# Kernel optimization log

Measured on AMD Instinct MI355X. Metric: run time of the kernel, lower is better.

The kernel has to match this reference:

```python
import jax, jax.numpy as jnp
import numpy as np

NUM_HEADS = 8
KEY_DIM = 32   # head_dim * attn_ratio(=1.0); head_dim = 256 // 8
SCALE = KEY_DIM ** -0.5


def qconv(x, w, groups, pad):
    """Quaternion (Hamilton product) conv. x: [B,C,4,H,W], w: [4,O,C//groups,kh,kw]."""
    B, C, Q, H, W = x.shape
    # fold the 4 quaternion components into the batch dim -> one conv per weight component
    xs = jnp.transpose(x, (0, 2, 1, 3, 4)).reshape(B * 4, C, H, W)
    ys = []
    for i in range(4):
        y = jax.lax.conv_general_dilated(
            xs, w[i], (1, 1), [(pad, pad), (pad, pad)],
            dimension_numbers=('NCHW', 'OIHW', 'NCHW'), feature_group_count=groups)
        ys.append(y.reshape(B, 4, y.shape[1], y.shape[2], y.shape[3]))
    yr, yi, yj, yk = ys  # y{w}[:, a] = conv(x_component_a, w_component_w)
    out_r = yr[:, 0] - yi[:, 1] - yj[:, 2] - yk[:, 3]
    out_i = yi[:, 0] + yr[:, 1] + yk[:, 2] - yj[:, 3]
    out_j = yj[:, 0] - yk[:, 1] + yr[:, 2] + yi[:, 3]
    out_k = yk[:, 0] + yj[:, 1] - yi[:, 2] + yr[:, 3]
    return jnp.stack([out_r, out_i, out_j, out_k], axis=2)  # [B,O,4,H,W]


def iqbn(x, gamma, beta, eps=1e-5):
    """Independent quaternion BN: per (channel, component) stats over (B,H,W)."""
    mean = x.mean(axis=(0, 3, 4), keepdims=True)
    var = x.var(axis=(0, 3, 4), keepdims=True)
    g = gamma[None, :, :, None, None]
    b = beta[None, :, :, None, None]
    return g * (x - mean) * jax.lax.rsqrt(var + eps) + b


def psablock(x, w_qkv, w_proj, w_pe, g_n, b_n, w_f1, g_f1, b_f1, w_f2, g_f2, b_f2):
    B, C, Q, H, W = x.shape
    N = H * W
    # --- QAttention ---
    qkv = qconv(x, w_qkv, 1, 0).reshape(B, NUM_HEADS, -1, 4, N)  # [B,nh,2kd+hd,4,N]
    q = qkv[:, :, :KEY_DIM]
    k = qkv[:, :, KEY_DIM:2 * KEY_DIM]
    v = qkv[:, :, 2 * KEY_DIM:]
    # channel attention: gram over spatial tokens N, softmax over channel dim d
    attn = jnp.einsum('bhcqn,bhdqn->bhqcd', q, k) * SCALE
    attn = jax.nn.softmax(attn, axis=-1)
    o = jnp.einsum('bhqcd,bhdqn->bhcqn', attn, v).reshape(B, C, 4, H, W)
    o = o + qconv(o, w_pe, C // 4, 1)   # depthwise-style 3x3 positional conv
    o = qconv(o, w_proj, 1, 0)
    o = iqbn(o, g_n, b_n)
    x = x + o  # shortcut
    # --- conv FFN ---
    f = qconv(x, w_f1, 1, 0)
    f = jax.nn.relu(iqbn(f, g_f1, b_f1))
    f = qconv(f, w_f2, 1, 0)
    f = iqbn(f, g_f2, b_f2)
    return x + f  # shortcut


def setup_inputs() -> dict:
    key = jax.random.key(0)
    ks = jax.random.split(key, 6)
    C, S = 256, 64
    return {
        'x': jax.random.normal(ks[0], (4, C, 4, S, S), jnp.float32),
        'w_qkv': jax.random.normal(ks[1], (4, 3 * C, C, 1, 1), jnp.float32) * 0.05,
        'w_proj': jax.random.normal(ks[2], (4, C, C, 1, 1), jnp.float32) * 0.05,
        'w_pe': jax.random.normal(ks[3], (4, C, 4, 3, 3), jnp.float32) * 0.05,
        'g_n': jnp.ones((C, 4), jnp.float32),
        'b_n': jnp.zeros((C, 4), jnp.float32),
        'w_f1': jax.random.normal(ks[4], (4, 2 * C, C, 1, 1), jnp.float32) * 0.05,
        'g_f1': jnp.ones((2 * C, 4), jnp.float32),
        'b_f1': jnp.zeros((2 * C, 4), jnp.float32),
        'w_f2': jax.random.normal(ks[5], (4, C, 2 * C, 1, 1), jnp.float32) * 0.05,
        'g_f2': jnp.ones((C, 4), jnp.float32),
        'b_f2': jnp.zeros((C, 4), jnp.float32),
    }


def reference(x, w_qkv, w_proj, w_pe, g_n, b_n, w_f1, g_f1, b_f1, w_f2, g_f2, b_f2):
    return psablock(x, w_qkv, w_proj, w_pe, g_n, b_n, w_f1, g_f1, b_f1, w_f2, g_f2, b_f2)
```

## Files before the change

### kernel.cpp

```cpp
#include <hip/hip_runtime.h>

typedef unsigned short u16;
typedef __bf16 bf16x8 __attribute__((ext_vector_type(8)));
typedef float f32x4 __attribute__((ext_vector_type(4)));

typedef const __attribute__((address_space(1))) void gv_t;
typedef __attribute__((address_space(3))) void lv_t;

__device__ __forceinline__ float b2f(u16 u) {
    union { unsigned int i; float f; } v; v.i = ((unsigned int)u) << 16; return v.f;
}
__device__ __forceinline__ u16 f2b(float f) {
    union { unsigned int i; float f; } v; v.f = f;
    unsigned int b = v.i;
    return (u16)((b + 0x7FFFu + ((b >> 16) & 1u)) >> 16);
}

__constant__ int   c_qidx[16] = {0,1,2,3, 1,0,3,2, 2,3,0,1, 3,2,1,0};
__constant__ float c_qsgn[16] = {1,-1,-1,-1, 1,1,1,-1, 1,-1,1,1, 1,1,-1,1};

__device__ __forceinline__ void frag_decode(long i, int KT, int& m, int& k) {
    int j = (int)(i & 7), r16 = (int)((i >> 3) & 15);
    int quad = (int)((i >> 7) & 3), frag = (int)((i >> 9) & 7);
    long t2 = i >> 12;
    int ktile = (int)(t2 % KT), mtile = (int)(t2 / KT);
    m = mtile * 128 + frag * 16 + r16;
    k = ktile * 32 + quad * 8 + j;
}
__device__ __forceinline__ u16 weff(const float* __restrict__ w, int OC, int Cin, int m, int k) {
    int o = m >> 2, p = m & 3, c = k >> 2, q = k & 3, pq = (p << 2) | q;
    return f2b(c_qsgn[pq] * w[c_qidx[pq] * OC + o * Cin + c]);
}

__global__ void build_weights(const float* __restrict__ wqkv, const float* __restrict__ wproj,
                              const float* __restrict__ wf1, const float* __restrict__ wf2,
                              const float* __restrict__ wpe,
                              u16* __restrict__ Wq, u16* __restrict__ Wp, u16* __restrict__ W1,
                              u16* __restrict__ W2, float* __restrict__ Wpe_eff)
{
    long i = (long)blockIdx.x * 256 + threadIdx.x;
    int m, k;
    if (i < 3145728L) {
        frag_decode(i, 32, m, k);
        Wq[i] = weff(wqkv, 196608, 256, m, k);
        return;
    }
    i -= 3145728L;
    if (i < 1048576L) {
        frag_decode(i, 32, m, k);
        Wp[i] = weff(wproj, 65536, 256, m, k);
        return;
    }
    i -= 1048576L;
    if (i < 2097152L) {
        frag_decode(i, 32, m, k);
        W1[i] = weff(wf1, 131072, 256, m, k);
        return;
    }
    i -= 2097152L;
    if (i < 2097152L) {
        frag_decode(i, 64, m, k);
        W2[i] = weff(wf2, 131072, 512, m, k);
        return;
    }
    i -= 2097152L;
    if (i < 147456L) {
        int g = (int)(i / 2304), r = (int)(i % 2304);
        int tap = r >> 8, r2 = r & 255;
        int fi = r2 >> 4, of = r2 & 15;
        int ol = of >> 2, p = of & 3, ci = fi >> 2, q = fi & 3, pq = (p << 2) | q;
        Wpe_eff[i] = c_qsgn[pq] * wpe[c_qidx[pq] * 9216 + (g * 4 + ol) * 36 + ci * 9 + tap];
    }
}

__global__ void zero_f(float* __restrict__ a)
{
    a[blockIdx.x * 256 + threadIdx.x] = 0.f;
}

__global__ __launch_bounds__(256) void cast_tr(const float* __restrict__ x, u16* __restrict__ Xt)
{
    int b = blockIdx.z, mt = blockIdx.y * 64, nt = blockIdx.x * 64;
    __shared__ u16 tl[64][66];
    int t = threadIdx.x, sub = t >> 4, c4 = (t & 15) * 4;
#pragma unroll
    for (int rr = 0; rr < 4; rr++) {
        int row = rr * 16 + sub;
        float4 v = *(const float4*)(x + ((long)b * 1024 + mt + row) * 4096 + nt + c4);
        uint2 pk;
        pk.x = (unsigned int)f2b(v.x) | ((unsigned int)f2b(v.y) << 16);
        pk.y = (unsigned int)f2b(v.z) | ((unsigned int)f2b(v.w) << 16);
        *(uint2*)(&tl[row][c4]) = pk;
    }
    __syncthreads();
#pragma unroll
    for (int rr = 0; rr < 4; rr++) {
        int row = rr * 16 + sub;
        uint2 o;
        o.x = (unsigned int)tl[c4][row] | ((unsigned int)tl[c4 + 1][row] << 16);
        o.y = (unsigned int)tl[c4 + 2][row] | ((unsigned int)tl[c4 + 3][row] << 16);
        *(uint2*)(Xt + ((long)b * 4096 + nt + row) * 1024 + mt + c4) = o;
    }
}

__device__ __forceinline__ void gl16(const u16* g, u16* l) {
    __builtin_amdgcn_global_load_lds((gv_t*)g, (lv_t*)l, 16, 0, 0);
}

template<int QM>
__device__ __forceinline__ void load_a(const u16* aS, bf16x8 (&afr)[4][2]) {
#pragma unroll
    for (int f = 0; f < 4; f++)
#pragma unroll
        for (int kk = 0; kk < 2; kk++)
            afr[f][kk] = *(const bf16x8*)(aS + (kk * 8 + QM * 4 + f) * 512);
}
template<int QN>
__device__ __forceinline__ void load_b(const u16* bS, bf16x8 (&bfr)[2][2]) {
#pragma unroll
    for (int g = 0; g < 2; g++)
#pragma unroll
        for (int kk = 0; kk < 2; kk++)
            bfr[g][kk] = *(const bf16x8*)(bS + (QN * 2 + g) * 1024 + kk * 512);
}
template<int QM, int QN>
__device__ __forceinline__ void mf16(const bf16x8 (&afr)[4][2], const bf16x8 (&bfr)[2][2],
                                     f32x4 (&acc)[8][4]) {
    __builtin_amdgcn_s_setprio(1);
#pragma unroll
    for (int f = 0; f < 4; f++)
#pragma unroll
        for (int g = 0; g < 2; g++)
#pragma unroll
            for (int kk = 0; kk < 2; kk++)
                acc[QM * 4 + f][QN * 2 + g] = __builtin_amdgcn_mfma_f32_16x16x32_bf16(
                    afr[f][kk], bfr[g][kk], acc[QM * 4 + f][QN * 2 + g], 0, 0, 0);
    __builtin_amdgcn_s_setprio(0);
}

#define PHASE_SYNC() \
    __builtin_amdgcn_sched_barrier(0); \
    asm volatile("s_waitcnt vmcnt(4)" ::: "memory"); \
    __builtin_amdgcn_s_barrier(); \
    asm volatile("s_waitcnt lgkmcnt(0)" ::: "memory"); \
    __builtin_amdgcn_sched_barrier(0);

template<bool TROUT>
__global__ __launch_bounds__(512, 2) void gemm256(
    const u16* __restrict__ A, const u16* __restrict__ Bt, u16* __restrict__ C,
    int M, int N, int K, long strideB, long strideC)
{
    __shared__ __align__(16) u16 smem[65536];
    const int t = threadIdx.x;
    const int b = blockIdx.z;
    const int m0 = blockIdx.y * 256, n0 = blockIdx.x * 256;
    const int l = t & 63, w = t >> 6;
    const int wr = w >> 2, wc = w & 3;
    const int quad = l >> 4, r16 = l & 15;
    const int KT32 = K >> 5, NT = K >> 6;
    const u16* Bb = Bt + (long)b * strideB;

    const u16* aB0 = A + (long)(2 * blockIdx.y) * KT32 * 4096 + t * 8;
    const u16* aB1 = aB0 + (long)KT32 * 4096;
    const int rowS = (w >> 1) * 16 + r16;
    const int colS = (w & 1) * 32 + quad * 8;
    const u16* bB0 = Bb + (long)(n0 + rowS) * K + colS;
    const u16* bB1 = bB0 + (long)128 * K;
    const long bStep = (long)64 * K;

    const int aOff = wr * 8192 + l * 8;
    const int bOff = 16384 + wc * 4096 + l * 8;

#define STAGE_A(ktv, h) { \
    const u16* s_ = ((h) ? aB1 : aB0) + (long)(ktv) * 8192; \
    u16* d_ = smem + (((ktv) & 1) * 32768) + (h) * 8192 + t * 8; \
    gl16(s_, d_); gl16(s_ + 4096, d_ + 4096); }
#define STAGE_B(ktv, h) { \
    const u16* s_ = ((h) ? bB1 : bB0) + (ktv) * 64; \
    u16* d_ = smem + (((ktv) & 1) * 32768) + 16384 + (h) * 8192 + t * 8; \
    gl16(s_, d_); gl16(s_ + bStep, d_ + 4096); }

    f32x4 acc[8][4];
#pragma unroll
    for (int i = 0; i < 8; i++)
#pragma unroll
        for (int j = 0; j < 4; j++) acc[i][j] = (f32x4){0.f, 0.f, 0.f, 0.f};

    bf16x8 RA[4][2], RB0[2][2], RB1[2][2];

    STAGE_B(0, 0); STAGE_A(0, 0); STAGE_B(0, 1); STAGE_A(0, 1);
    STAGE_B(1, 0); STAGE_A(1, 0);
    asm volatile("s_waitcnt vmcnt(4)" ::: "memory");
    __builtin_amdgcn_s_barrier();

    for (int kt = 0; kt < NT; ++kt) {
        const int so = (kt & 1) * 32768;
        const u16* aS = smem + so + aOff;
        const u16* bS = smem + so + bOff;
        const int k1 = (kt + 1 < NT) ? kt + 1 : NT - 1;
        const int k2 = (kt + 2 < NT) ? kt + 2 : NT - 1;

        load_a<0>(aS, RA);
        load_b<0>(bS, RB0);
        STAGE_B(k1, 1);
        PHASE_SYNC();
        mf16<0, 0>(RA, RB0, acc);
        __builtin_amdgcn_s_barrier();
        load_b<1>(bS, RB1);
        STAGE_A(k1, 1);
        PHASE_SYNC();
        mf16<0, 1>(RA, RB1, acc);
        __builtin_amdgcn_s_barrier();
        load_a<1>(aS, RA);
        STAGE_B(k2, 0);
        PHASE_SYNC();
        mf16<1, 1>(RA, RB1, acc);
        __builtin_amdgcn_s_barrier();
        STAGE_A(k2, 0);
        PHASE_SYNC();
        mf16<1, 0>(RA, RB0, acc);
        __builtin_amdgcn_s_barrier();
    }
    asm volatile("s_waitcnt vmcnt(0)" ::: "memory");
    __builtin_amdgcn_s_barrier();
#undef STAGE_A
#undef STAGE_B

    if (!TROUT) {
        u16* Cb = C + (long)b * strideC;
#pragma unroll
        for (int i = 0; i < 8; i++)
#pragma unroll
            for (int j = 0; j < 4; j++) {
                int mm = m0 + wr * 128 + i * 16 + quad * 4;
                int nn = n0 + wc * 64 + j * 16 + r16;
#pragma unroll
                for (int r = 0; r < 4; r++)
                    Cb[(long)(mm + r) * N + nn] = f2b(acc[i][j][r]);
            }
    } else {
        u16* Ct = smem;
        u16* Cb = C + (long)b * strideC;
#pragma unroll
        for (int h = 0; h < 2; h++) {
            __syncthreads();
            if ((wc >> 1) == h) {
#pragma unroll
                for (int i = 0; i < 8; i++)
#pragma unroll
                    for (int j = 0; j < 4; j++) {
                        int nn = (wc & 1) * 64 + j * 16 + r16;
                        int mm = wr * 128 + i * 16 + quad * 4;
                        ushort4 pk;
                        pk.x = f2b(acc[i][j][0]); pk.y = f2b(acc[i][j][1]);
                        pk.z = f2b(acc[i][j][2]); pk.w = f2b(acc[i][j][3]);
                        *(ushort4*)(Ct + nn * 264 + mm) = pk;
                    }
            }
            __syncthreads();
#pragma unroll
            for (int e = 0; e < 8; e++) {
                int idx = e * 512 + t;
                int n = idx >> 5, m8 = (idx & 31) * 8;
                uint4 v = *(const uint4*)(Ct + n * 264 + m8);
                *(uint4*)(Cb + (long)(n0 + h * 128 + n) * M + m0 + m8) = v;
            }
        }
    }
}
#undef PHASE_SYNC

__global__ __launch_bounds__(256) void attn_s(const u16* __restrict__ QKV, float* __restrict__ S)
{
    const int chunk = blockIdx.x, bhp = blockIdx.y;
    const int bi = bhp >> 5, h = (bhp >> 2) & 7, p = bhp & 3;
    const long rs = 16384;
    const u16* base = QKV + (long)bi * (3072L * 4096) + (long)(h * 384 + p) * 4096;
    const int t = threadIdx.x, l = t & 63, w = t >> 6;
    const int quad = l >> 4, r16 = l & 15;
    __shared__ float Sred[4][32][32];

    f32x4 acc[2][2];
#pragma unroll
    for (int i = 0; i < 2; i++)
#pragma unroll
        for (int j = 0; j < 2; j++) acc[i][j] = (f32x4){0.f, 0.f, 0.f, 0.f};

    const int nb = chunk * 1024 + w * 256 + quad * 8;
    for (int kk = 0; kk < 256; kk += 32) {
        long off = nb + kk;
        bf16x8 q0 = *(const bf16x8*)(base + (long)r16 * rs + off);
        bf16x8 q1 = *(const bf16x8*)(base + (long)(16 + r16) * rs + off);
        bf16x8 k0 = *(const bf16x8*)(base + (long)(32 + r16) * rs + off);
        bf16x8 k1 = *(const bf16x8*)(base + (long)(48 + r16) * rs + off);
        acc[0][0] = __builtin_amdgcn_mfma_f32_16x16x32_bf16(q0, k0, acc[0][0], 0, 0, 0);
        acc[0][1] = __builtin_amdgcn_mfma_f32_16x16x32_bf16(q0, k1, acc[0][1], 0, 0, 0);
        acc[1][0] = __builtin_amdgcn_mfma_f32_16x16x32_bf16(q1, k0, acc[1][0], 0, 0, 0);
        acc[1][1] = __builtin_amdgcn_mfma_f32_16x16x32_bf16(q1, k1, acc[1][1], 0, 0, 0);
    }
#pragma unroll
    for (int i = 0; i < 2; i++)
#pragma unroll
        for (int j = 0; j < 2; j++)
#pragma unroll
            for (int r = 0; r < 4; r++)
                Sred[w][i * 16 + quad * 4 + r][j * 16 + r16] = acc[i][j][r];
    __syncthreads();
    for (int e = t; e < 1024; e += 256) {
        int c = e >> 5, d = e & 31;
        float v = Sred[0][c][d] + Sred[1][c][d] + Sred[2][c][d] + Sred[3][c][d];
        atomicAdd(&S[(long)bhp * 1024 + e], v);
    }
}

__global__ __launch_bounds__(256) void attn_pv(const u16* __restrict__ QKV, const float* __restrict__ S,
                                               u16* __restrict__ O)
{
    const int ns = blockIdx.x * 512, bhp = blockIdx.y;
    const int bi = bhp >> 5, h = (bhp >> 2) & 7, p = bhp & 3;
    const long rs = 16384;
    const u16* base = QKV + (long)bi * (3072L * 4096) + (long)(h * 384 + p) * 4096;
    const int t = threadIdx.x;
    __shared__ float Pl[1024];
    for (int e = t; e < 1024; e += 256) Pl[e] = S[(long)bhp * 1024 + e];
    __syncthreads();
    if (t < 32) {
        float r[32];
        float mx = -1e30f;
#pragma unroll
        for (int d = 0; d < 32; d++) { r[d] = Pl[t * 32 + d] * 0.17677669529663687f; mx = fmaxf(mx, r[d]); }
        float sum = 0.f;
#pragma unroll
        for (int d = 0; d < 32; d++) { r[d] = __expf(r[d] - mx); sum += r[d]; }
        float inv = 1.f / sum;
#pragma unroll
        for (int d = 0; d < 32; d++) Pl[t * 32 + d] = r[d] * inv;
    }
    __syncthreads();

    float v[32][2];
#pragma unroll
    for (int d = 0; d < 32; d++) {
        unsigned int u = *(const unsigned int*)(base + (long)(64 + d) * rs + ns + 2 * t);
        v[d][0] = b2f((u16)u); v[d][1] = b2f((u16)(u >> 16));
    }
    u16* Ob = O + (long)bi * (1024L * 4096) + (long)(h * 128 + p) * 4096;
    for (int c = 0; c < 32; c++) {
        float s0 = 0.f, s1 = 0.f;
        const float4* prow = (const float4*)(&Pl[c * 32]);
#pragma unroll
        for (int dq = 0; dq < 8; dq++) {
            float4 pv = prow[dq];
            s0 = fmaf(pv.x, v[4*dq+0][0], s0); s1 = fmaf(pv.x, v[4*dq+0][1], s1);
            s0 = fmaf(pv.y, v[4*dq+1][0], s0); s1 = fmaf(pv.y, v[4*dq+1][1], s1);
            s0 = fmaf(pv.z, v[4*dq+2][0], s0); s1 = fmaf(pv.z, v[4*dq+2][1], s1);
            s0 = fmaf(pv.w, v[4*dq+3][0], s0); s1 = fmaf(pv.w, v[4*dq+3][1], s1);
        }
        *(unsigned int*)(Ob + (long)c * 16384 + ns + 2 * t) =
            (unsigned int)f2b(s0) | ((unsigned int)f2b(s1) << 16);
    }
}

__global__ __launch_bounds__(256) void pe_kernel(const u16* __restrict__ Oin,
                                                 const float* __restrict__ Wpe,
                                                 u16* __restrict__ O2t)
{
    const int tile = blockIdx.x, g = blockIdx.y, bi = blockIdx.z;
    const int y0 = (tile >> 2) * 16, x0 = (tile & 3) * 16;
    __shared__ float tin[16][324];
    const int t = threadIdx.x;
    const u16* Ob = Oin + (long)bi * (1024L * 4096) + (long)(g * 16) * 4096;
    for (int e = t; e < 16 * 324; e += 256) {
        int f = e / 324, rem = e % 324;
        int yy = rem / 18 - 1 + y0, xx = rem % 18 - 1 + x0;
        float v = 0.f;
        if (yy >= 0 && yy < 64 && xx >= 0 && xx < 64)
            v = b2f(Ob[(long)f * 4096 + yy * 64 + xx]);
        tin[f][rem] = v;
    }
    __syncthreads();
    const int y = t >> 4, x = t & 15;
    float acc[16];
#pragma unroll
    for (int of = 0; of < 16; of++) acc[of] = tin[of][(y + 1) * 18 + (x + 1)];
    const float* Wg = Wpe + g * 2304;
    for (int dy = 0; dy < 3; dy++)
        for (int dx = 0; dx < 3; dx++) {
            int off = (y + dy) * 18 + (x + dx);
            int tap = dy * 3 + dx;
            for (int fi = 0; fi < 16; fi++) {
                float v = tin[fi][off];
                const float* wp = Wg + (tap * 16 + fi) * 16;
#pragma unroll
                for (int of = 0; of < 16; of++) acc[of] = fmaf(wp[of], v, acc[of]);
            }
        }
    long n = (long)(y0 + y) * 64 + (x0 + x);
    unsigned int* op = (unsigned int*)(O2t + ((long)bi * 4096 + n) * 1024 + g * 16);
#pragma unroll
    for (int u = 0; u < 8; u++)
        op[u] = (unsigned int)f2b(acc[2 * u]) | ((unsigned int)f2b(acc[2 * u + 1]) << 16);
}

__global__ __launch_bounds__(256) void bn_stats(const u16* __restrict__ X, float* __restrict__ stats, int M)
{
    const int m = blockIdx.x, t = threadIdx.x;
    float s = 0.f, ss = 0.f;
    for (int b = 0; b < 4; b++) {
        const u16* rowp = X + ((long)b * M + m) * 4096;
        for (int pass = 0; pass < 2; pass++) {
            uint4 uv = *(const uint4*)(rowp + pass * 2048 + t * 8);
            unsigned int wsa[4] = {uv.x, uv.y, uv.z, uv.w};
#pragma unroll
            for (int u = 0; u < 4; u++) {
                float v0 = b2f((u16)wsa[u]), v1 = b2f((u16)(wsa[u] >> 16));
                s += v0 + v1; ss += v0 * v0 + v1 * v1;
            }
        }
    }
    __shared__ float rs[4], rss[4];
    for (int o = 32; o > 0; o >>= 1) { s += __shfl_down(s, o); ss += __shfl_down(ss, o); }
    if ((t & 63) == 0) { rs[t >> 6] = s; rss[t >> 6] = ss; }
    __syncthreads();
    if (t == 0) {
        float S = rs[0] + rs[1] + rs[2] + rs[3];
        float SS = rss[0] + rss[1] + rss[2] + rss[3];
        float mean = S * (1.f / 16384.f);
        float var = SS * (1.f / 16384.f) - mean * mean;
        stats[2 * m] = mean;
        stats[2 * m + 1] = rsqrtf(var + 1e-5f);
    }
}

__global__ __launch_bounds__(256) void bn_add_tr(const float* __restrict__ x, const u16* __restrict__ P,
    const float* __restrict__ stats, const float* __restrict__ gamma, const float* __restrict__ beta,
    u16* __restrict__ X1t)
{
    int b = blockIdx.z, mt = blockIdx.y * 64, nt = blockIdx.x * 64;
    __shared__ u16 tl[64][66];
    int t = threadIdx.x, sub = t >> 4, c4 = (t & 15) * 4;
#pragma unroll
    for (int rr = 0; rr < 4; rr++) {
        int row = rr * 16 + sub, m = mt + row;
        float gm = gamma[m] * stats[2 * m + 1];
        float bs = beta[m] - gm * stats[2 * m];
        long gi = ((long)b * 1024 + m) * 4096 + nt + c4;
        float4 xv = *(const float4*)(x + gi);
        uint2 pv = *(const uint2*)(P + gi);
        uint2 pk;
        pk.x = (unsigned int)f2b(xv.x + fmaf(gm, b2f((u16)pv.x), bs)) |
               ((unsigned int)f2b(xv.y + fmaf(gm, b2f((u16)(pv.x >> 16)), bs)) << 16);
        pk.y = (unsigned int)f2b(xv.z + fmaf(gm, b2f((u16)pv.y), bs)) |
               ((unsigned int)f2b(xv.w + fmaf(gm, b2f((u16)(pv.y >> 16)), bs)) << 16);
        *(uint2*)(&tl[row][c4]) = pk;
    }
    __syncthreads();
#pragma unroll
    for (int rr = 0; rr < 4; rr++) {
        int row = rr * 16 + sub;
        uint2 o;
        o.x = (unsigned int)tl[c4][row] | ((unsigned int)tl[c4 + 1][row] << 16);
        o.y = (unsigned int)tl[c4 + 2][row] | ((unsigned int)tl[c4 + 3][row] << 16);
        *(uint2*)(X1t + ((long)b * 4096 + nt + row) * 1024 + mt + c4) = o;
    }
}

__global__ __launch_bounds__(256) void bn_stats_col(const u16* __restrict__ Xp, float* __restrict__ accum)
{
    const int t = threadIdx.x;
    const int f0 = t * 8;
    float s[8], ss[8];
#pragma unroll
    for (int u = 0; u < 8; u++) { s[u] = 0.f; ss[u] = 0.f; }
    const u16* base = Xp + (long)blockIdx.x * 128 * 2048;
    for (int r = 0; r < 128; r++) {
        uint4 uv = *(const uint4*)(base + (long)r * 2048 + f0);
        unsigned int wsa[4] = {uv.x, uv.y, uv.z, uv.w};
#pragma unroll
        for (int u = 0; u < 4; u++) {
            float v0 = b2f((u16)wsa[u]), v1 = b2f((u16)(wsa[u] >> 16));
            s[2*u] += v0;   ss[2*u]   += v0 * v0;
            s[2*u+1] += v1; ss[2*u+1] += v1 * v1;
        }
    }
#pragma unroll
    for (int u = 0; u < 8; u++) {
        atomicAdd(&accum[f0 + u], s[u]);
        atomicAdd(&accum[2048 + f0 + u], ss[u]);
    }
}

__global__ __launch_bounds__(256) void bn_relu_ip(u16* __restrict__ Xp, const float* __restrict__ accum,
    const float* __restrict__ gamma, const float* __restrict__ beta)
{
    long i = ((long)blockIdx.x * 256 + threadIdx.x) * 8;
    int f = (int)(i & 2047);
    uint4 uv = *(const uint4*)(Xp + i);
    unsigned int wsa[4] = {uv.x, uv.y, uv.z, uv.w};
    unsigned int ov[4];
#pragma unroll
    for (int u = 0; u < 4; u++) {
        unsigned int o = 0;
#pragma unroll
        for (int h = 0; h < 2; h++) {
            int ff = f + 2 * u + h;
            float S = accum[ff], SS = accum[2048 + ff];
            float mean = S * (1.f / 16384.f);
            float var = SS * (1.f / 16384.f) - mean * mean;
            float g = gamma[ff] * rsqrtf(var + 1e-5f);
            float bb = beta[ff] - g * mean;
            float xv = b2f((u16)(wsa[u] >> (16 * h)));
            float v = fmaxf(fmaf(g, xv, bb), 0.f);
            o |= ((unsigned int)f2b(v)) << (16 * h);
        }
        ov[u] = o;
    }
    *(uint4*)(Xp + i) = *(uint4*)ov;
}

__global__ __launch_bounds__(256) void final_tr(const u16* __restrict__ X1t, const u16* __restrict__ F2,
    const float* __restrict__ stats, const float* __restrict__ gamma, const float* __restrict__ beta,
    float* __restrict__ out)
{
    int b = blockIdx.z, mt = blockIdx.y * 64, nt = blockIdx.x * 64;
    __shared__ u16 tl[64][66];
    int t = threadIdx.x, sub = t >> 4, c4 = (t & 15) * 4;
#pragma unroll
    for (int rr = 0; rr < 4; rr++) {
        int row = rr * 16 + sub;
        uint2 v = *(const uint2*)(X1t + ((long)b * 4096 + nt + row) * 1024 + mt + c4);
        *(uint2*)(&tl[row][c4]) = v;
    }
    __syncthreads();
#pragma unroll
    for (int rr = 0; rr < 4; rr++) {
        int row = rr * 16 + sub, m = mt + row;
        float gm = gamma[m] * stats[2 * m + 1];
        float bs = beta[m] - gm * stats[2 * m];
        long gi = ((long)b * 1024 + m) * 4096 + nt + c4;
        uint2 f = *(const uint2*)(F2 + gi);
        float4 o;
        o.x = b2f(tl[c4][row])     + fmaf(gm, b2f((u16)f.x), bs);
        o.y = b2f(tl[c4 + 1][row]) + fmaf(gm, b2f((u16)(f.x >> 16)), bs);
        o.z = b2f(tl[c4 + 2][row]) + fmaf(gm, b2f((u16)f.y), bs);
        o.w = b2f(tl[c4 + 3][row]) + fmaf(gm, b2f((u16)(f.y >> 16)), bs);
        *(float4*)(out + gi) = o;
    }
}

extern "C" void kernel_launch(void* const* d_in, const int* in_sizes, int n_in,
                              void* d_out, int out_size, void* d_ws, size_t ws_size,
                              hipStream_t stream)
{
    const float* x     = (const float*)d_in[0];
    const float* wqkv  = (const float*)d_in[1];
    const float* wproj = (const float*)d_in[2];
    const float* wpe   = (const float*)d_in[3];
    const float* g_n   = (const float*)d_in[4];
    const float* b_n   = (const float*)d_in[5];
    const float* wf1   = (const float*)d_in[6];
    const float* g_f1  = (const float*)d_in[7];
    const float* b_f1  = (const float*)d_in[8];
    const float* wf2   = (const float*)d_in[9];
    const float* g_f2  = (const float*)d_in[10];
    const float* b_f2  = (const float*)d_in[11];
    float* out = (float*)d_out;
    char* ws = (char*)d_ws;

    u16*   Wq      = (u16*)(ws + 0);
    u16*   Wp      = (u16*)(ws + 6291456);
    u16*   W1      = (u16*)(ws + 8388608);
    u16*   W2      = (u16*)(ws + 12582912);
    float* Wpe_eff = (float*)(ws + 16777216);
    float* st1     = (float*)(ws + 17367040);
    float* accum2  = (float*)(ws + 17375232);
    float* Sbuf    = (float*)(ws + 17391616);
    float* st3     = (float*)(ws + 17915904);
    u16*   QKV = (u16*)(ws + 17924096);
    u16*   O2t = (u16*)(ws + 17924096);
    u16*   X1t = (u16*)(ws + 17924096);
    u16*   P   = (u16*)(ws + 51478528);
    u16*   F1p = (u16*)(ws + 51478528);
    u16*   Xt  = (u16*)(ws + 118587392);
    u16*   Oat = (u16*)(ws + 118587392);
    u16*   F2  = (u16*)(ws + 118587392);

    zero_f<<<528, 256, 0, stream>>>(accum2);
    build_weights<<<33344, 256, 0, stream>>>(wqkv, wproj, wf1, wf2, wpe, Wq, Wp, W1, W2, Wpe_eff);
    cast_tr<<<dim3(64, 16, 4), 256, 0, stream>>>(x, Xt);
    gemm256<false><<<dim3(16, 12, 4), 512, 0, stream>>>(Wq, Xt, QKV, 3072, 4096, 1024, 4096L * 1024, 3072L * 4096);
    attn_s<<<dim3(4, 128), 256, 0, stream>>>(QKV, Sbuf);
    attn_pv<<<dim3(8, 128), 256, 0, stream>>>(QKV, Sbuf, Oat);
    pe_kernel<<<dim3(16, 64, 4), 256, 0, stream>>>(Oat, Wpe_eff, O2t);
    gemm256<false><<<dim3(16, 4, 4), 512, 0, stream>>>(Wp, O2t, P, 1024, 4096, 1024, 4096L * 1024, 1024L * 4096);
    bn_stats<<<1024, 256, 0, stream>>>(P, st1, 1024);
    bn_add_tr<<<dim3(64, 16, 4), 256, 0, stream>>>(x, P, st1, g_n, b_n, X1t);
    gemm256<true><<<dim3(16, 8, 4), 512, 0, stream>>>(W1, X1t, F1p, 2048, 4096, 1024, 4096L * 1024, 4096L * 2048);
    bn_stats_col<<<128, 256, 0, stream>>>(F1p, accum2);
    bn_relu_ip<<<16384, 256, 0, stream>>>(F1p, accum2, g_f1, b_f1);
    gemm256<false><<<dim3(16, 4, 4), 512, 0, stream>>>(W2, F1p, F2, 1024, 4096, 2048, 4096L * 2048, 1024L * 4096);
    bn_stats<<<1024, 256, 0, stream>>>(F2, st3, 1024);
    final_tr<<<dim3(64, 16, 4), 256, 0, stream>>>(X1t, F2, st3, g_f2, b_f2, out);
}
```

Measured before the change: 693.3 us.

## Run grouped 3x3 positional conv on MFMA and fuse prologue kernels

Three prologue kernels (zeroing, weight building, input cast/transpose) are merged into one launch to cut launch overhead. The positional 3x3 grouped conv is rewritten as a small bf16 MFMA GEMM: weights are prepacked as bf16 fragments with K padded from 144 to 160. The input tile is staged in shared memory channel-innermost, replacing the scalar fp32 FMA loop. Conv weights are now bf16 rather than fp32, which slightly lowers precision.

```diff
diff --git a/kernel.cpp b/kernel.cpp
--- a/kernel.cpp
+++ b/kernel.cpp
@@ -32,57 +32,71 @@
     return f2b(c_qsgn[pq] * w[c_qidx[pq] * OC + o * Cin + c]);
 }
 
-__global__ void build_weights(const float* __restrict__ wqkv, const float* __restrict__ wproj,
-                              const float* __restrict__ wf1, const float* __restrict__ wf2,
-                              const float* __restrict__ wpe,
-                              u16* __restrict__ Wq, u16* __restrict__ Wp, u16* __restrict__ W1,
-                              u16* __restrict__ W2, float* __restrict__ Wpe_eff)
-{
-    long i = (long)blockIdx.x * 256 + threadIdx.x;
-    int m, k;
-    if (i < 3145728L) {
-        frag_decode(i, 32, m, k);
-        Wq[i] = weff(wqkv, 196608, 256, m, k);
+__global__ __launch_bounds__(256) void prologue(
+    const float* __restrict__ x,
+    const float* __restrict__ wqkv, const float* __restrict__ wproj,
+    const float* __restrict__ wf1, const float* __restrict__ wf2,
+    const float* __restrict__ wpe,
+    float* __restrict__ zbuf,
+    u16* __restrict__ Wq, u16* __restrict__ Wp, u16* __restrict__ W1,
+    u16* __restrict__ W2, u16* __restrict__ Wpe16,
+    u16* __restrict__ Xt)
+{
+    const int bid = blockIdx.x;
+    const int t = threadIdx.x;
+    __shared__ u16 tl[64][66];
+
+    if (bid < 528) {
+        zbuf[bid * 256 + t] = 0.f;
         return;
     }
-    i -= 3145728L;
-    if (i < 1048576L) {
-        frag_decode(i, 32, m, k);
-        Wp[i] = weff(wproj, 65536, 256, m, k);
+    if (bid < 33936) {
+        long i = (long)(bid - 528) * 256 + t;
+        int m, k;
+        if (i < 3145728L) {
+            frag_decode(i, 32, m, k);
+            Wq[i] = weff(wqkv, 196608, 256, m, k);
+            return;
+        }
+        i -= 3145728L;
+        if (i < 1048576L) {
+            frag_decode(i, 32, m, k);
+            Wp[i] = weff(wproj, 65536, 256, m, k);
+            return;
+        }
+        i -= 1048576L;
+        if (i < 2097152L) {
+            frag_decode(i, 32, m, k);
+            W1[i] = weff(wf1, 131072, 256, m, k);
+            return;
+        }
+        i -= 2097152L;
+        if (i < 2097152L) {
+            frag_decode(i, 64, m, k);
+            W2[i] = weff(wf2, 131072, 512, m, k);
+            return;
+        }
+        i -= 2097152L;
+        if (i < 163840L) {
+            int j = (int)(i & 7), of = (int)((i >> 3) & 15);
+            int quad = (int)((i >> 7) & 3);
+            int blk = (int)(i >> 9);
+            int kt = blk % 5, g = blk / 5;
+            int kk = kt * 32 + quad * 8 + j;
+            int tap = kk >> 4, fi = kk & 15;
+            u16 val = 0;
+            if (tap < 9) {
+                int ol = of >> 2, p = of & 3, ci = fi >> 2, q = fi & 3;
+                int pq = (p << 2) | q;
+                val = f2b(c_qsgn[pq] * wpe[c_qidx[pq] * 9216 + (g * 4 + ol) * 36 + ci * 9 + tap]);
+            }
+            Wpe16[i] = val;
+        }
         return;
     }
-    i -= 1048576L;
-    if (i < 2097152L) {
-        frag_decode(i, 32, m, k);
-        W1[i] = weff(wf1, 131072, 256, m, k);
-        return;
-    }
-    i -= 2097152L;
-    if (i < 2097152L) {
-        frag_decode(i, 64, m, k);
-        W2[i] = weff(wf2, 131072, 512, m, k);
-        return;
-    }
-    i -= 2097152L;
-    if (i < 147456L) {
-        int g = (int)(i / 2304), r = (int)(i % 2304);
-        int tap = r >> 8, r2 = r & 255;
-        int fi = r2 >> 4, of = r2 & 15;
-        int ol = of >> 2, p = of & 3, ci = fi >> 2, q = fi & 3, pq = (p << 2) | q;
-        Wpe_eff[i] = c_qsgn[pq] * wpe[c_qidx[pq] * 9216 + (g * 4 + ol) * 36 + ci * 9 + tap];
-    }
-}
-
-__global__ void zero_f(float* __restrict__ a)
-{
-    a[blockIdx.x * 256 + threadIdx.x] = 0.f;
-}
-
-__global__ __launch_bounds__(256) void cast_tr(const float* __restrict__ x, u16* __restrict__ Xt)
-{
-    int b = blockIdx.z, mt = blockIdx.y * 64, nt = blockIdx.x * 64;
-    __shared__ u16 tl[64][66];
-    int t = threadIdx.x, sub = t >> 4, c4 = (t & 15) * 4;
+    int c = bid - 33936;
+    int b = c >> 10, mt = ((c >> 6) & 15) * 64, nt = (c & 63) * 64;
+    int sub = t >> 4, c4 = (t & 15) * 4;
 #pragma unroll
     for (int rr = 0; rr < 4; rr++) {
         int row = rr * 16 + sub;
@@ -362,44 +376,56 @@
 }
 
 __global__ __launch_bounds__(256) void pe_kernel(const u16* __restrict__ Oin,
-                                                 const float* __restrict__ Wpe,
+                                                 const u16* __restrict__ Wpe,
                                                  u16* __restrict__ O2t)
 {
     const int tile = blockIdx.x, g = blockIdx.y, bi = blockIdx.z;
     const int y0 = (tile >> 2) * 16, x0 = (tile & 3) * 16;
-    __shared__ float tin[16][324];
+    __shared__ u16 tin2[324][24];
     const int t = threadIdx.x;
     const u16* Ob = Oin + (long)bi * (1024L * 4096) + (long)(g * 16) * 4096;
-    for (int e = t; e < 16 * 324; e += 256) {
-        int f = e / 324, rem = e % 324;
+    for (int e = t; e < 4 * 324; e += 256) {
+        int f0 = (e / 324) * 4, rem = e % 324;
         int yy = rem / 18 - 1 + y0, xx = rem % 18 - 1 + x0;
-        float v = 0.f;
-        if (yy >= 0 && yy < 64 && xx >= 0 && xx < 64)
-            v = b2f(Ob[(long)f * 4096 + yy * 64 + xx]);
-        tin[f][rem] = v;
-    }
-    __syncthreads();
-    const int y = t >> 4, x = t & 15;
-    float acc[16];
-#pragma unroll
-    for (int of = 0; of < 16; of++) acc[of] = tin[of][(y + 1) * 18 + (x + 1)];
-    const float* Wg = Wpe + g * 2304;
-    for (int dy = 0; dy < 3; dy++)
-        for (int dx = 0; dx < 3; dx++) {
-            int off = (y + dy) * 18 + (x + dx);
-            int tap = dy * 3 + dx;
-            for (int fi = 0; fi < 16; fi++) {
-                float v = tin[fi][off];
-                const float* wp = Wg + (tap * 16 + fi) * 16;
-#pragma unroll
-                for (int of = 0; of < 16; of++) acc[of] = fmaf(wp[of], v, acc[of]);
-            }
-        }
-    long n = (long)(y0 + y) * 64 + (x0 + x);
-    unsigned int* op = (unsigned int*)(O2t + ((long)bi * 4096 + n) * 1024 + g * 16);
-#pragma unroll
-    for (int u = 0; u < 8; u++)
-        op[u] = (unsigned int)f2b(acc[2 * u]) | ((unsigned int)f2b(acc[2 * u + 1]) << 16);
+        ushort4 v = {0, 0, 0, 0};
+        if (yy >= 0 && yy < 64 && xx >= 0 && xx < 64) {
+            long o = (long)yy * 64 + xx;
+            v.x = Ob[(long)(f0 + 0) * 4096 + o];
+            v.y = Ob[(long)(f0 + 1) * 4096 + o];
+            v.z = Ob[(long)(f0 + 2) * 4096 + o];
+            v.w = Ob[(long)(f0 + 3) * 4096 + o];
+        }
+        *(ushort4*)(&tin2[rem][f0]) = v;
+    }
+    __syncthreads();
+
+    const int l = t & 63, w = t >> 6;
+    const int quad = l >> 4, r16 = l & 15;
+    const u16* Wg = Wpe + g * 2560;
+    bf16x8 af[5];
+#pragma unroll
+    for (int kt = 0; kt < 5; kt++)
+        af[kt] = *(const bf16x8*)(Wg + kt * 512 + quad * 128 + r16 * 8);
+
+    const int tap_base = quad >> 1, fi0 = (quad & 1) * 8;
+#pragma unroll
+    for (int i = 0; i < 4; i++) {
+        int y = w * 4 + i;
+        const u16* rc = &tin2[(y + 1) * 18 + (r16 + 1)][quad * 4];
+        f32x4 acc;
+        acc[0] = b2f(rc[0]); acc[1] = b2f(rc[1]); acc[2] = b2f(rc[2]); acc[3] = b2f(rc[3]);
+#pragma unroll
+        for (int kt = 0; kt < 5; kt++) {
+            int tap = kt * 2 + tap_base;
+            int sp = (tap < 9) ? (y + tap / 3) * 18 + (r16 + tap % 3) : 0;
+            bf16x8 bf = *(const bf16x8*)(&tin2[sp][fi0]);
+            acc = __builtin_amdgcn_mfma_f32_16x16x32_bf16(af[kt], bf, acc, 0, 0, 0);
+        }
+        long n = (long)(y0 + y) * 64 + (x0 + r16);
+        ushort4 pk;
+        pk.x = f2b(acc[0]); pk.y = f2b(acc[1]); pk.z = f2b(acc[2]); pk.w = f2b(acc[3]);
+        *(ushort4*)(O2t + ((long)bi * 4096 + n) * 1024 + g * 16 + quad * 4) = pk;
+    }
 }
 
 __global__ __launch_bounds__(256) void bn_stats(const u16* __restrict__ X, float* __restrict__ stats, int M)
@@ -571,7 +597,7 @@
     u16*   Wp      = (u16*)(ws + 6291456);
     u16*   W1      = (u16*)(ws + 8388608);
     u16*   W2      = (u16*)(ws + 12582912);
-    float* Wpe_eff = (float*)(ws + 16777216);
+    u16*   Wpe16   = (u16*)(ws + 16777216);
     float* st1     = (float*)(ws + 17367040);
     float* accum2  = (float*)(ws + 17375232);
     float* Sbuf    = (float*)(ws + 17391616);
@@ -585,13 +611,12 @@
     u16*   Oat = (u16*)(ws + 118587392);
     u16*   F2  = (u16*)(ws + 118587392);
 
-    zero_f<<<528, 256, 0, stream>>>(accum2);
-    build_weights<<<33344, 256, 0, stream>>>(wqkv, wproj, wf1, wf2, wpe, Wq, Wp, W1, W2, Wpe_eff);
-    cast_tr<<<dim3(64, 16, 4), 256, 0, stream>>>(x, Xt);
+    prologue<<<38032, 256, 0, stream>>>(x, wqkv, wproj, wf1, wf2, wpe,
+                                        accum2, Wq, Wp, W1, W2, Wpe16, Xt);
     gemm256<false><<<dim3(16, 12, 4), 512, 0, stream>>>(Wq, Xt, QKV, 3072, 4096, 1024, 4096L * 1024, 3072L * 4096);
     attn_s<<<dim3(4, 128), 256, 0, stream>>>(QKV, Sbuf);
     attn_pv<<<dim3(8, 128), 256, 0, stream>>>(QKV, Sbuf, Oat);
-    pe_kernel<<<dim3(16, 64, 4), 256, 0, stream>>>(Oat, Wpe_eff, O2t);
+    pe_kernel<<<dim3(16, 64, 4), 256, 0, stream>>>(Oat, Wpe16, O2t);
     gemm256<false><<<dim3(16, 4, 4), 512, 0, stream>>>(Wp, O2t, P, 1024, 4096, 1024, 4096L * 1024, 1024L * 4096);
     bn_stats<<<1024, 256, 0, stream>>>(P, st1, 1024);
     bn_add_tr<<<dim3(64, 16, 4), 256, 0, stream>>>(x, P, st1, g_n, b_n, X1t);
```

Result: faster. 606.2 us (-12.6%).
